# Optimization experiments

Measured on AMD Instinct MI355X. Metric: run time of the kernel, lower is better.

Reference implementation:

```python
import jax, jax.numpy as jnp
import numpy as np

H = 128  # hidden_size

def _band_agg(h):
    # Equivalent to bmm(adj, h) with adj = degree-normalized tridiagonal
    # (self + left + right neighbor), degree=3 interior, 2 at endpoints,
    # normalization adj/(deg+1e-8) as in the torch module.
    B, S, D = h.shape
    hp = jnp.pad(h, ((0, 0), (1, 1), (0, 0)))
    s = hp[:, :-2] + hp[:, 1:-1] + hp[:, 2:]            # [B,S,D] neighbor sum
    deg = jnp.full((S,), 3.0, dtype=h.dtype).at[0].set(2.0).at[S - 1].set(2.0)
    return s / (deg + 1e-8)[None, :, None]


def setup_inputs() -> dict:
    key = jax.random.key(0)
    ks = jax.random.split(key, 16)
    f32 = jnp.float32
    p = lambda k, shp: (jax.random.normal(k, shp, dtype=f32) * 0.05)
    return {
        "x": jax.random.normal(ks[0], (32, 2048, 6), dtype=f32),
        "enc_w1": p(ks[1], (6, H)),   "enc_b1": p(ks[2], (H,)),
        "enc_w2": p(ks[3], (H, H)),   "enc_b2": p(ks[4], (H,)),
        "gc1_w": p(ks[5], (H, H)),    "gc1_b": p(ks[6], (H,)),
        "gc2_w": p(ks[7], (H, H)),    "gc2_b": p(ks[8], (H,)),
        "gc3_w": p(ks[9], (H, H)),    "gc3_b": p(ks[10], (H,)),
        "cls_w1": p(ks[11], (H, H // 2)), "cls_b1": p(ks[12], (H // 2,)),
        "cls_w2": p(ks[13], (H // 2, 3)), "cls_b2": p(ks[14], (3,)),
    }


def reference(x, enc_w1, enc_b1, enc_w2, enc_b2,
              gc1_w, gc1_b, gc2_w, gc2_b, gc3_w, gc3_b,
              cls_w1, cls_b1, cls_w2, cls_b2):
    # node encoder: Linear -> ReLU -> Linear
    h = jax.nn.relu(x @ enc_w1 + enc_b1) @ enc_w2 + enc_b2
    # three graph convolutions: linear, normalized tridiagonal aggregate, relu
    h = jax.nn.relu(_band_agg(h @ gc1_w + gc1_b))
    h = jax.nn.relu(_band_agg(h @ gc2_w + gc2_b))
    h = jax.nn.relu(_band_agg(h @ gc3_w + gc3_b))
    # AdaptiveAvgPool1d(1) over seq dim after transpose == mean over nodes
    pooled = h.mean(axis=1)                              # [B, H]
    # classifier (dropout inactive in eval)
    return jax.nn.relu(pooled @ cls_w1 + cls_b1) @ cls_w2 + cls_b2
```

## Files before the change

kernel.cpp:

```cpp
#include <hip/hip_runtime.h>

#define SEQ  2048
#define HID  128
#define NB   32
#define TILE 58
#define GX   36
#define MSTR 67

typedef float f2    __attribute__((ext_vector_type(2)));
typedef float f32x4 __attribute__((ext_vector_type(4)));
typedef short bf16x8 __attribute__((ext_vector_type(8)));

__device__ __forceinline__ void split_bf16(float v, short& h, short& l) {
  unsigned u = __float_as_uint(v);
  unsigned r = (u + 0x7fffu + ((u >> 16) & 1u)) >> 16;
  h = (short)r;
  const float hf = __uint_as_float(r << 16);
  const float lo = v - hf;
  unsigned u2 = __float_as_uint(lo);
  unsigned r2 = (u2 + 0x7fffu + ((u2 >> 16) & 1u)) >> 16;
  l = (short)r2;
}

__global__ __launch_bounds__(256) void prep_kernel(
    const float* __restrict__ enc_w2, const float* __restrict__ enc_b2,
    const float* __restrict__ gc1_w, const float* __restrict__ gc1_b,
    const float* __restrict__ gc2_w, const float* __restrict__ gc3_w,
    short* __restrict__ Wf, float* __restrict__ bp)
{
  __shared__ float Wls[32][130];
  __shared__ float ew2s[32][128];
  __shared__ float bsum[2][128];

  const int ks = blockIdx.x;
  const int L  = blockIdx.y;
  const int tid = threadIdx.x;

  if (L == 0) {
    for (int f = tid; f < 32 * 128; f += 256)
      ew2s[f >> 7][f & 127] = enc_w2[(ks * 32 + (f >> 7)) * 128 + (f & 127)];
    __syncthreads();
    {
      const int c = tid & 127, rh = tid >> 7;
      float acc[16];
      #pragma unroll
      for (int i = 0; i < 16; ++i) acc[i] = 0.f;
      #pragma unroll 4
      for (int k = 0; k < 128; ++k) {
        const float g = gc1_w[k * 128 + c];
        #pragma unroll
        for (int i = 0; i < 16; ++i)
          acc[i] = fmaf(ew2s[rh * 16 + i][k], g, acc[i]);
      }
      #pragma unroll
      for (int i = 0; i < 16; ++i) Wls[rh * 16 + i][c] = acc[i];
    }
    if (ks == 0) {
      const int c = tid & 127, kh = tid >> 7;
      float s = 0.f;
      #pragma unroll 4
      for (int k0 = 0; k0 < 64; ++k0) {
        const int k = kh * 64 + k0;
        s = fmaf(enc_b2[k], gc1_w[k * 128 + c], s);
      }
      bsum[kh][c] = s;
    }
    __syncthreads();
    if (ks == 0 && tid < 128) bp[tid] = gc1_b[tid] + bsum[0][tid] + bsum[1][tid];
  } else {
    const float* SW = (L == 1) ? gc2_w : gc3_w;
    for (int f = tid; f < 32 * 128; f += 256)
      Wls[f >> 7][f & 127] = SW[(ks * 32 + (f >> 7)) * 128 + (f & 127)];
    __syncthreads();
  }

  short* hi = Wf + L * 32768 + ks * 4096;
  short* lo = hi + 16384;
  for (int f = tid; f < 4096; f += 256) {
    const int nt = f >> 9, l = (f >> 3) & 63, j = f & 7;
    const int kk = (l >> 4) * 8 + j;
    const int n  = nt * 16 + (l & 15);
    short h, lw;
    split_bf16(Wls[kk][n], h, lw);
    hi[f] = h; lo[f] = lw;
  }
}

__global__ __launch_bounds__(256) void fused_kernel(
    const float* __restrict__ x,
    const float* __restrict__ enc_w1, const float* __restrict__ enc_b1,
    const short* __restrict__ Wf, const float* __restrict__ bp,
    const float* __restrict__ gc2_b, const float* __restrict__ gc3_b,
    float* __restrict__ partial)
{
  __shared__ float hT[HID * MSTR];
  __shared__ float wsmall[7 * HID];
  __shared__ float psum[256];

  const int tid  = threadIdx.x;
  const int lane = tid & 63;
  const int w    = tid >> 6;
  const int gxb  = blockIdx.x, b = blockIdx.y;
  const int s0   = gxb * TILE;

  for (int f = tid; f < 7 * HID; f += 256)
    wsmall[f] = (f < 6 * HID) ? enc_w1[f] : enc_b1[f - 6 * HID];

  const int sm = s0 - 3 + lane;
  float xv[6];
  if (sm >= 0 && sm < SEQ) {
    const f2* xp = (const f2*)(x + ((long long)b * SEQ + sm) * 6);
    const f2 a0 = xp[0], a1 = xp[1], a2 = xp[2];
    xv[0] = a0.x; xv[1] = a0.y; xv[2] = a1.x;
    xv[3] = a1.y; xv[4] = a2.x; xv[5] = a2.y;
  } else {
    #pragma unroll
    for (int k = 0; k < 6; ++k) xv[k] = 0.f;
  }
  __syncthreads();
  {
    const int c0 = w * 32;
    float4 a4[8];
    #pragma unroll
    for (int q = 0; q < 8; ++q) a4[q] = make_float4(0.f, 0.f, 0.f, 0.f);
    #pragma unroll
    for (int k = 0; k < 6; ++k) {
      #pragma unroll
      for (int q = 0; q < 8; ++q) {
        const float4 wv = *(const float4*)&wsmall[k * HID + c0 + q * 4];
        a4[q].x = fmaf(xv[k], wv.x, a4[q].x);
        a4[q].y = fmaf(xv[k], wv.y, a4[q].y);
        a4[q].z = fmaf(xv[k], wv.z, a4[q].z);
        a4[q].w = fmaf(xv[k], wv.w, a4[q].w);
      }
    }
    #pragma unroll
    for (int q = 0; q < 8; ++q) {
      const float4 bb = *(const float4*)&wsmall[6 * HID + c0 + q * 4];
      const int c = c0 + q * 4;
      hT[(c + 0) * MSTR + lane] = fmaxf(a4[q].x + bb.x, 0.f);
      hT[(c + 1) * MSTR + lane] = fmaxf(a4[q].y + bb.y, 0.f);
      hT[(c + 2) * MSTR + lane] = fmaxf(a4[q].z + bb.z, 0.f);
      hT[(c + 3) * MSTR + lane] = fmaxf(a4[q].w + bb.w, 0.f);
    }
  }
  __syncthreads();

  const int mt   = w * 16 + (lane & 15);
  const int koct = (lane >> 4) * 8;
  const int stt  = s0 - 3 + mt;
  const float invdA = (stt == 0 || stt == SEQ - 1) ? (1.0f / (2.0f + 1e-8f))
                                                   : (1.0f / (3.0f + 1e-8f));
  const int mm = (mt == 0) ? 0 : mt - 1;
  const int mp = (mt == 63) ? 63 : mt + 1;

  #pragma unroll 1
  for (int L = 0; L < 3; ++L) {
    const short* WfL = Wf + L * 32768;
    const bf16x8* Bhi = (const bf16x8*)WfL;
    const bf16x8* Blo = (const bf16x8*)(WfL + 16384);
    const float* bias = (L == 0) ? bp : (L == 1) ? gc2_b : gc3_b;

    f32x4 acc[8];
    #pragma unroll
    for (int nt = 0; nt < 8; ++nt) acc[nt] = (f32x4){0.f, 0.f, 0.f, 0.f};

    #pragma unroll 1
    for (int ks = 0; ks < 4; ++ks) {
      const int fb = ks * 512 + lane;
      bf16x8 bh[8], bl[8];
      #pragma unroll
      for (int nt = 0; nt < 8; ++nt) {
        bh[nt] = Bhi[fb + nt * 64];
        bl[nt] = Blo[fb + nt * 64];
      }
      bf16x8 ah, al;
      const float* pa = &hT[(ks * 32 + koct) * MSTR];
      #pragma unroll
      for (int j = 0; j < 8; ++j) {
        float v;
        if (L == 0) {
          v = pa[j * MSTR + mt];
        } else {
          v = (pa[j * MSTR + mm] + pa[j * MSTR + mt] + pa[j * MSTR + mp]) * invdA;
          v = fmaxf(v, 0.f);
        }
        short h, lo;
        split_bf16(v, h, lo);
        ah[j] = h; al[j] = lo;
      }
      #pragma unroll
      for (int nt = 0; nt < 8; ++nt) {
        acc[nt] = __builtin_amdgcn_mfma_f32_16x16x32_bf16(ah, bh[nt], acc[nt], 0, 0, 0);
        acc[nt] = __builtin_amdgcn_mfma_f32_16x16x32_bf16(ah, bl[nt], acc[nt], 0, 0, 0);
        acc[nt] = __builtin_amdgcn_mfma_f32_16x16x32_bf16(al, bh[nt], acc[nt], 0, 0, 0);
      }
    }
    __syncthreads();

    {
      const int n0 = lane & 15;
      const int mrow0 = w * 16 + (lane >> 4) * 4;
      #pragma unroll
      for (int nt = 0; nt < 8; ++nt) {
        const float bn = bias[nt * 16 + n0];
        float* pw = &hT[(nt * 16 + n0) * MSTR];
        #pragma unroll
        for (int r = 0; r < 4; ++r) {
          const int m = mrow0 + r;
          const int s = s0 - 3 + m;
          const bool vld = (s >= 0 && s < SEQ);
          pw[m] = vld ? (acc[nt][r] + bn) : 0.f;
        }
      }
    }
    __syncthreads();
  }

  {
    const int c = tid & 127, half = tid >> 7;
    float ps = 0.f;
    const float* pc = &hT[c * MSTR];
    #pragma unroll 1
    for (int r = 0; r < 29; ++r) {
      const int m = 3 + half * 29 + r;
      const int s = s0 + half * 29 + r;
      if (s < SEQ) {
        const float invd = (s == 0 || s == SEQ - 1) ? (1.0f / (2.0f + 1e-8f))
                                                    : (1.0f / (3.0f + 1e-8f));
        ps += fmaxf((pc[m - 1] + pc[m] + pc[m + 1]) * invd, 0.f);
      }
    }
    psum[tid] = ps;
  }
  __syncthreads();
  if (tid < 128)
    partial[((long long)b * GX + gxb) * HID + tid] = psum[tid] + psum[tid + 128];
}

__global__ __launch_bounds__(256) void cls_kernel(
    const float* __restrict__ partial,
    const float* __restrict__ w1, const float* __restrict__ b1,
    const float* __restrict__ w2, const float* __restrict__ b2,
    float* __restrict__ out)
{
  __shared__ float red[256];
  __shared__ float ms[128];
  __shared__ float hp[4][64];
  __shared__ float hid[64];
  const int b = blockIdx.x, tid = threadIdx.x;

  {
    const int c = tid & 127, gh = tid >> 7;
    float a = 0.f;
    #pragma unroll 2
    for (int g = gh; g < GX; g += 2)
      a += partial[((long long)b * GX + g) * HID + c];
    red[tid] = a;
  }
  __syncthreads();
  if (tid < 128) ms[tid] = (red[tid] + red[tid + 128]) * (1.0f / 2048.0f);
  __syncthreads();

  {
    const int c = tid & 63, kq = tid >> 6;
    float h = 0.f;
    #pragma unroll 8
    for (int k0 = 0; k0 < 32; ++k0) {
      const int k = kq * 32 + k0;
      h = fmaf(ms[k], w1[k * 64 + c], h);
    }
    hp[kq][c] = h;
  }
  __syncthreads();
  if (tid < 64)
    hid[tid] = fmaxf(hp[0][tid] + hp[1][tid] + hp[2][tid] + hp[3][tid] + b1[tid], 0.f);
  __syncthreads();

  if (tid < 3) {
    float o = b2[tid];
    #pragma unroll 8
    for (int k = 0; k < 64; ++k) o = fmaf(hid[k], w2[k * 3 + tid], o);
    out[b * 3 + tid] = o;
  }
}

extern "C" void kernel_launch(void* const* d_in, const int* in_sizes, int n_in,
                              void* d_out, int out_size, void* d_ws, size_t ws_size,
                              hipStream_t stream) {
  (void)in_sizes; (void)n_in; (void)out_size; (void)ws_size;
  const float* x      = (const float*)d_in[0];
  const float* enc_w1 = (const float*)d_in[1];
  const float* enc_b1 = (const float*)d_in[2];
  const float* enc_w2 = (const float*)d_in[3];
  const float* enc_b2 = (const float*)d_in[4];
  const float* gc1_w  = (const float*)d_in[5];
  const float* gc1_b  = (const float*)d_in[6];
  const float* gc2_w  = (const float*)d_in[7];
  const float* gc2_b  = (const float*)d_in[8];
  const float* gc3_w  = (const float*)d_in[9];
  const float* gc3_b  = (const float*)d_in[10];
  const float* cls_w1 = (const float*)d_in[11];
  const float* cls_b1 = (const float*)d_in[12];
  const float* cls_w2 = (const float*)d_in[13];
  const float* cls_b2 = (const float*)d_in[14];

  short* Wfrag   = (short*)d_ws;
  float* bpv     = (float*)(Wfrag + 3 * 2 * 16384);
  float* partial = bpv + 128;

  prep_kernel<<<dim3(4, 3), 256, 0, stream>>>(
      enc_w2, enc_b2, gc1_w, gc1_b, gc2_w, gc3_w, Wfrag, bpv);
  fused_kernel<<<dim3(GX, NB), 256, 0, stream>>>(
      x, enc_w1, enc_b1, Wfrag, bpv, gc2_b, gc3_b, partial);
  cls_kernel<<<dim3(NB), 256, 0, stream>>>(partial, cls_w1, cls_b1, cls_w2, cls_b2,
                                           (float*)d_out);
}
```

Baseline: 151.4 us.

## Precompute split-bf16 MFMA A-fragments in shared memory once per layer

Instead of every MFMA A-fragment load recomputing the tridiagonal aggregate, ReLU and bf16 hi/lo split from a transposed float tile, each layer's output is aggregated and split once into fragment-ordered hi/lo bf16 buffers. The GEMM loop then does two vector LDS loads per k-step. Shared memory is laid out row-major with vectorized float4 neighbor reads, and the final pooling uses a sliding window. The lo part is now truncated rather than rounded, which slightly changes numerics. An extra barrier per layer is added.

New measurement: 168.7 us. +11.4%, slower.

```diff
diff --git a/kernel.cpp b/kernel.cpp
--- a/kernel.cpp
+++ b/kernel.cpp
@@ -5,21 +5,20 @@
 #define NB   32
 #define TILE 58
 #define GX   36
-#define MSTR 67
-
-typedef float f2    __attribute__((ext_vector_type(2)));
-typedef float f32x4 __attribute__((ext_vector_type(4)));
+#define TSTR 132
+#define RSTR 2080
+
+typedef float f2     __attribute__((ext_vector_type(2)));
+typedef float f32x4  __attribute__((ext_vector_type(4)));
 typedef short bf16x8 __attribute__((ext_vector_type(8)));
+typedef short s4v    __attribute__((ext_vector_type(4)));
 
 __device__ __forceinline__ void split_bf16(float v, short& h, short& l) {
   unsigned u = __float_as_uint(v);
   unsigned r = (u + 0x7fffu + ((u >> 16) & 1u)) >> 16;
   h = (short)r;
-  const float hf = __uint_as_float(r << 16);
-  const float lo = v - hf;
-  unsigned u2 = __float_as_uint(lo);
-  unsigned r2 = (u2 + 0x7fffu + ((u2 >> 16) & 1u)) >> 16;
-  l = (short)r2;
+  const float lo = v - __uint_as_float(r << 16);
+  l = (short)(__float_as_uint(lo) >> 16);
 }
 
 __global__ __launch_bounds__(256) void prep_kernel(
@@ -93,15 +92,19 @@
     const float* __restrict__ gc2_b, const float* __restrict__ gc3_b,
     float* __restrict__ partial)
 {
-  __shared__ float hT[HID * MSTR];
-  __shared__ float wsmall[7 * HID];
-  __shared__ float psum[256];
+  __shared__ __align__(16) float smem[8448 + 8320];
+  float* tbuf = smem;
+  short* fh   = (short*)(smem + 8448);
+  short* fl   = fh + 4 * RSTR;
+  float* wsmall = smem;
+  float* psum   = smem + 8448;
 
   const int tid  = threadIdx.x;
   const int lane = tid & 63;
   const int w    = tid >> 6;
   const int gxb  = blockIdx.x, b = blockIdx.y;
   const int s0   = gxb * TILE;
+  const float inv2 = 1.0f / (2.0f + 1e-8f), inv3 = 1.0f / (3.0f + 1e-8f);
 
   for (int f = tid; f < 7 * HID; f += 256)
     wsmall[f] = (f < 6 * HID) ? enc_w1[f] : enc_b1[f - 6 * HID];
@@ -134,25 +137,32 @@
         a4[q].w = fmaf(xv[k], wv.w, a4[q].w);
       }
     }
-    #pragma unroll
-    for (int q = 0; q < 8; ++q) {
-      const float4 bb = *(const float4*)&wsmall[6 * HID + c0 + q * 4];
-      const int c = c0 + q * 4;
-      hT[(c + 0) * MSTR + lane] = fmaxf(a4[q].x + bb.x, 0.f);
-      hT[(c + 1) * MSTR + lane] = fmaxf(a4[q].y + bb.y, 0.f);
-      hT[(c + 2) * MSTR + lane] = fmaxf(a4[q].z + bb.z, 0.f);
-      hT[(c + 3) * MSTR + lane] = fmaxf(a4[q].w + bb.w, 0.f);
-    }
-  }
-  __syncthreads();
-
-  const int mt   = w * 16 + (lane & 15);
-  const int koct = (lane >> 4) * 8;
-  const int stt  = s0 - 3 + mt;
-  const float invdA = (stt == 0 || stt == SEQ - 1) ? (1.0f / (2.0f + 1e-8f))
-                                                   : (1.0f / (3.0f + 1e-8f));
-  const int mm = (mt == 0) ? 0 : mt - 1;
-  const int mp = (mt == 63) ? 63 : mt + 1;
+    short* fhW = fh + (lane >> 4) * RSTR + w * 512;
+    short* flW = fl + (lane >> 4) * RSTR + w * 512;
+    #pragma unroll
+    for (int oct = 0; oct < 4; ++oct) {
+      float v[8];
+      #pragma unroll
+      for (int h = 0; h < 2; ++h) {
+        const int q = 2 * oct + h;
+        const float4 bb = *(const float4*)&wsmall[6 * HID + c0 + q * 4];
+        v[4*h+0] = fmaxf(a4[q].x + bb.x, 0.f);
+        v[4*h+1] = fmaxf(a4[q].y + bb.y, 0.f);
+        v[4*h+2] = fmaxf(a4[q].z + bb.z, 0.f);
+        v[4*h+3] = fmaxf(a4[q].w + bb.w, 0.f);
+      }
+      bf16x8 hs, ls;
+      #pragma unroll
+      for (int j = 0; j < 8; ++j) { short hh, ll; split_bf16(v[j], hh, ll); hs[j] = hh; ls[j] = ll; }
+      const int off = (((lane & 15) | (oct << 4))) * 8;
+      *(bf16x8*)(fhW + off) = hs;
+      *(bf16x8*)(flW + off) = ls;
+    }
+  }
+  __syncthreads();
+
+  const int n0 = lane & 15;
+  const int mrow0 = w * 16 + (lane >> 4) * 4;
 
   #pragma unroll 1
   for (int L = 0; L < 3; ++L) {
@@ -174,21 +184,9 @@
         bh[nt] = Bhi[fb + nt * 64];
         bl[nt] = Blo[fb + nt * 64];
       }
-      bf16x8 ah, al;
-      const float* pa = &hT[(ks * 32 + koct) * MSTR];
-      #pragma unroll
-      for (int j = 0; j < 8; ++j) {
-        float v;
-        if (L == 0) {
-          v = pa[j * MSTR + mt];
-        } else {
-          v = (pa[j * MSTR + mm] + pa[j * MSTR + mt] + pa[j * MSTR + mp]) * invdA;
-          v = fmaxf(v, 0.f);
-        }
-        short h, lo;
-        split_bf16(v, h, lo);
-        ah[j] = h; al[j] = lo;
-      }
+      const int fa = w * RSTR + ks * 512 + lane * 8;
+      const bf16x8 ah = *(const bf16x8*)(fh + fa);
+      const bf16x8 al = *(const bf16x8*)(fl + fa);
       #pragma unroll
       for (int nt = 0; nt < 8; ++nt) {
         acc[nt] = __builtin_amdgcn_mfma_f32_16x16x32_bf16(ah, bh[nt], acc[nt], 0, 0, 0);
@@ -198,38 +196,64 @@
     }
     __syncthreads();
 
-    {
-      const int n0 = lane & 15;
-      const int mrow0 = w * 16 + (lane >> 4) * 4;
-      #pragma unroll
-      for (int nt = 0; nt < 8; ++nt) {
-        const float bn = bias[nt * 16 + n0];
-        float* pw = &hT[(nt * 16 + n0) * MSTR];
+    #pragma unroll
+    for (int nt = 0; nt < 8; ++nt) {
+      const float bn = bias[nt * 16 + n0];
+      #pragma unroll
+      for (int r = 0; r < 4; ++r) {
+        const int m = mrow0 + r;
+        const int s = s0 - 3 + m;
+        const bool vld = (s >= 0 && s < SEQ);
+        tbuf[m * TSTR + nt * 16 + n0] = vld ? (acc[nt][r] + bn) : 0.f;
+      }
+    }
+    __syncthreads();
+
+    if (L < 2) {
+      #pragma unroll
+      for (int i = 0; i < 8; ++i) {
+        const int task = i * 256 + tid;
+        const int m = task >> 5, kq = task & 31, k0 = kq * 4;
+        const int mm = (m == 0) ? 0 : m - 1;
+        const int mp = (m == 63) ? 63 : m + 1;
+        const float4 A = *(const float4*)&tbuf[mm * TSTR + k0];
+        const float4 Bv = *(const float4*)&tbuf[m  * TSTR + k0];
+        const float4 Cv = *(const float4*)&tbuf[mp * TSTR + k0];
+        const int s = s0 - 3 + m;
+        const float invd = (s == 0 || s == SEQ - 1) ? inv2 : inv3;
+        float v[4];
+        v[0] = fmaxf((A.x + Bv.x + Cv.x) * invd, 0.f);
+        v[1] = fmaxf((A.y + Bv.y + Cv.y) * invd, 0.f);
+        v[2] = fmaxf((A.z + Bv.z + Cv.z) * invd, 0.f);
+        v[3] = fmaxf((A.w + Bv.w + Cv.w) * invd, 0.f);
+        s4v hs, ls;
         #pragma unroll
-        for (int r = 0; r < 4; ++r) {
-          const int m = mrow0 + r;
-          const int s = s0 - 3 + m;
-          const bool vld = (s >= 0 && s < SEQ);
-          pw[m] = vld ? (acc[nt][r] + bn) : 0.f;
-        }
-      }
-    }
-    __syncthreads();
+        for (int j = 0; j < 4; ++j) { short hh, ll; split_bf16(v[j], hh, ll); hs[j] = hh; ls[j] = ll; }
+        const int base = (m >> 4) * RSTR + (kq >> 3) * 512 +
+                         (((m & 15) | (((kq >> 1) & 3) << 4))) * 8 + (kq & 1) * 4;
+        *(s4v*)(fh + base) = hs;
+        *(s4v*)(fl + base) = ls;
+      }
+      __syncthreads();
+    }
   }
 
   {
-    const int c = tid & 127, half = tid >> 7;
+    const int c = tid & 127, g2 = tid >> 7;
+    const int mstart = 3 + g2 * 29;
+    float prev = tbuf[(mstart - 1) * TSTR + c];
+    float cur  = tbuf[mstart * TSTR + c];
     float ps = 0.f;
-    const float* pc = &hT[c * MSTR];
     #pragma unroll 1
     for (int r = 0; r < 29; ++r) {
-      const int m = 3 + half * 29 + r;
-      const int s = s0 + half * 29 + r;
+      const int m = mstart + r;
+      const int s = s0 + g2 * 29 + r;
+      const float nxt = tbuf[(m + 1) * TSTR + c];
       if (s < SEQ) {
-        const float invd = (s == 0 || s == SEQ - 1) ? (1.0f / (2.0f + 1e-8f))
-                                                    : (1.0f / (3.0f + 1e-8f));
-        ps += fmaxf((pc[m - 1] + pc[m] + pc[m + 1]) * invd, 0.f);
-      }
+        const float invd = (s == 0 || s == SEQ - 1) ? inv2 : inv3;
+        ps += fmaxf((prev + cur + nxt) * invd, 0.f);
+      }
+      prev = cur; cur = nxt;
     }
     psum[tid] = ps;
   }
@@ -261,7 +285,6 @@
   __syncthreads();
   if (tid < 128) ms[tid] = (red[tid] + red[tid + 128]) * (1.0f / 2048.0f);
   __syncthreads();
-
   {
     const int c = tid & 63, kq = tid >> 6;
     float h = 0.f;
@@ -276,7 +299,6 @@
   if (tid < 64)
     hid[tid] = fmaxf(hp[0][tid] + hp[1][tid] + hp[2][tid] + hp[3][tid] + b1[tid], 0.f);
   __syncthreads();
-
   if (tid < 3) {
     float o = b2[tid];
     #pragma unroll 8
```
